# Performance work log

Measured on AMD Instinct MI355X. Metric: run time of the kernel, lower is better.

## Reference

```python
import jax, jax.numpy as jnp
import numpy as np

NUM_ENTS = 1000
NUM_RELS = 100
HIDDEN = 200
N_QUERY = 50000
N_HIST = 1000000
ALPHA = 0.5


def setup_inputs() -> dict:
    key = jax.random.key(0)
    ks = jax.random.split(key, 12)
    s = 0.05  # small init for numerical stability (xavier-like scale)
    return {
        "ent_emb": jax.random.normal(ks[0], (NUM_ENTS, HIDDEN), jnp.float32) * s,
        "rel_emb": jax.random.normal(ks[1], (NUM_RELS, HIDDEN), jnp.float32) * s,
        "tim_emb": jax.random.normal(ks[2], (1, HIDDEN), jnp.float32) * s,
        "g_w": jax.random.normal(ks[3], (3 * HIDDEN, HIDDEN), jnp.float32) * s,
        "g_b": jnp.zeros((HIDDEN,), jnp.float32),
        "c_w": jax.random.normal(ks[4], (3 * HIDDEN, HIDDEN), jnp.float32) * s,
        "c_b": jnp.zeros((HIDDEN,), jnp.float32),
        "hist_sub": jax.random.randint(ks[5], (N_HIST,), 0, NUM_ENTS, jnp.int32),
        "hist_rel": jax.random.randint(ks[6], (N_HIST,), 0, NUM_RELS, jnp.int32),
        "hist_obj": jax.random.randint(ks[7], (N_HIST,), 0, NUM_ENTS, jnp.int32),
        "sub": jax.random.randint(ks[8], (N_QUERY,), 0, NUM_ENTS, jnp.int32),
        "rel": jax.random.randint(ks[9], (N_QUERY,), 0, NUM_RELS, jnp.int32),
    }


def reference(ent_emb, rel_emb, tim_emb, g_w, g_b, c_w, c_b,
              hist_sub, hist_rel, hist_obj, sub, rel):
    E = ent_emb.shape[0]
    R = rel_emb.shape[0]
    N = sub.shape[0]
    # Triple-count histogram over all history graphs (fused scatter-add;
    # equivalent to the per-graph python loop vocab[s,r,o] += 1).
    vocab = jnp.zeros((E, R, E), jnp.float32).at[hist_sub, hist_rel, hist_obj].add(1.0)
    # Query features: [N, 3H]
    x = jnp.concatenate(
        [ent_emb[sub], rel_emb[rel], jnp.broadcast_to(tim_emb, (N, tim_emb.shape[1]))],
        axis=1)
    # Generate-mode score distribution
    gscore = jax.nn.softmax(x @ g_w + g_b, axis=1)  # [N, H]
    # Copy-mode mask: 1 where the (sub, rel) pair occurred in history
    mask = (vocab[sub, rel].sum(axis=1, keepdims=True) != 0).astype(x.dtype)  # [N, 1]
    cscore = jax.nn.softmax(jnp.tanh(x @ c_w + c_b) + mask, axis=1)  # [N, H]
    fscore = gscore + ALPHA * (cscore - gscore)
    return jnp.log(fscore)
```

## Files before the change

kernel.cpp:

```cpp
#include <hip/hip_runtime.h>
#include <math.h>

#define HIDDEN 200
#define LOG2E 1.4426950408889634f
#define LN2   0.6931471805599453f

typedef float f32x4 __attribute__((ext_vector_type(4)));

__global__ __launch_bounds__(256) void precompute_kernel(
    const float* __restrict__ ent, const float* __restrict__ rel,
    const float* __restrict__ tim,
    const float* __restrict__ g_w, const float* __restrict__ g_b,
    const float* __restrict__ c_w, const float* __restrict__ c_b,
    float* __restrict__ EA, float* __restrict__ EB) {
  const int mode = blockIdx.y;
  const float* w = mode ? c_w : g_w;
  const float* bias = mode ? c_b : g_b;
  const bool is_ent = blockIdx.x < 500;
  const int row0 = is_ent ? blockIdx.x * 2 : (blockIdx.x - 500) * 2;
  const float* in = is_ent ? ent : rel;
  const int k0 = is_ent ? 0 : 200;
  float* obase = is_ent ? (EA + row0 * 400 + mode * 200)
                        : (EB + row0 * 400 + mode * 200);

  __shared__ float a0[HIDDEN], a1[HIDDEN], tl[HIDDEN];
  const int c = threadIdx.x;
  if (c < HIDDEN) {
    a0[c] = in[row0 * HIDDEN + c];
    a1[c] = in[(row0 + 1) * HIDDEN + c];
    if (!is_ent) tl[c] = tim[c];
  }
  __syncthreads();
  if (c >= HIDDEN) return;

  const float* wp = w + k0 * HIDDEN + c;
  float acc0a = 0.f, acc0b = 0.f, acc1a = 0.f, acc1b = 0.f;
  #pragma unroll 4
  for (int k = 0; k < 100; ++k) {
    float w0 = wp[k * HIDDEN];
    float w1 = wp[(k + 100) * HIDDEN];
    acc0a += a0[k] * w0;
    acc0b += a0[k + 100] * w1;
    acc1a += a1[k] * w0;
    acc1b += a1[k + 100] * w1;
  }
  float r0 = acc0a + acc0b;
  float r1 = acc1a + acc1b;
  if (!is_ent) {
    const float* wt = w + 400 * HIDDEN + c;
    float ta = 0.f, tb = 0.f;
    #pragma unroll 4
    for (int k = 0; k < 100; ++k) {
      ta += tl[k] * wt[k * HIDDEN];
      tb += tl[k + 100] * wt[(k + 100) * HIDDEN];
    }
    float extra = ta + tb + bias[c];
    r0 += extra;
    r1 += extra;
  }
  if (mode == 0) {
    r0 = __builtin_amdgcn_exp2f(r0 * LOG2E);
    r1 = __builtin_amdgcn_exp2f(r1 * LOG2E);
  }
  obase[c] = r0;
  obase[400 + c] = r1;
}

__global__ __launch_bounds__(128) void pair_kernel(
    const float* __restrict__ EA, const float* __restrict__ EB,
    float* __restrict__ SG, float* __restrict__ SC) {
  const int s = blockIdx.x;
  __shared__ float row[400];
  for (int i = threadIdx.x; i < 400; i += 128) row[i] = EA[s * 400 + i];
  __syncthreads();
  const int r = threadIdx.x;
  if (r >= 100) return;

  const float* ebg = EB + r * 400;
  const float* ebc = ebg + 200;
  float sg = 0.f, sc = 0.f;
  #pragma unroll 4
  for (int k = 0; k < 200; ++k) {
    sg = fmaf(row[k], ebg[k], sg);
    float x = row[200 + k] + ebc[k];
    float e2 = __builtin_amdgcn_exp2f(x * (2.f * LOG2E));
    float th = (e2 - 1.f) * __builtin_amdgcn_rcpf(e2 + 1.f);
    sc += __builtin_amdgcn_exp2f(th * LOG2E);
  }
  SG[s * 100 + r] = sg;
  SC[s * 100 + r] = sc;
}

__global__ __launch_bounds__(256) void query_kernel(
    const float* __restrict__ EA, const float* __restrict__ EB,
    const float* __restrict__ SG, const float* __restrict__ SC,
    const int* __restrict__ sub, const int* __restrict__ rel,
    float* __restrict__ out, int total) {
  int t = blockIdx.x * blockDim.x + threadIdx.x;
  if (t >= total) return;
  unsigned q = (unsigned)t / 50u;
  unsigned j = (unsigned)t - q * 50u;

  int s = sub[q];
  int r = rel[q];
  float isg = 0.5f * __builtin_amdgcn_rcpf(SG[s * 100 + r]);
  float isc = 0.5f * __builtin_amdgcn_rcpf(SC[s * 100 + r]);

  const f32x4* ea = (const f32x4*)(EA + s * 400);
  const f32x4* eb = (const f32x4*)(EB + r * 400);
  f32x4 eg = ea[j] * eb[j];
  f32x4 xc = ea[j + 50] + eb[j + 50];

  f32x4 o;
  #pragma unroll
  for (int i = 0; i < 4; ++i) {
    float e2 = __builtin_amdgcn_exp2f(xc[i] * (2.f * LOG2E));
    float th = (e2 - 1.f) * __builtin_amdgcn_rcpf(e2 + 1.f);
    float ec = __builtin_amdgcn_exp2f(th * LOG2E);
    float v = fmaf(eg[i], isg, ec * isc);
    o[i] = __builtin_amdgcn_logf(v) * LN2;
  }
  __builtin_nontemporal_store(o, (f32x4*)out + t);
}

extern "C" void kernel_launch(void* const* d_in, const int* in_sizes, int n_in,
                              void* d_out, int out_size, void* d_ws, size_t ws_size,
                              hipStream_t stream) {
  const float* ent  = (const float*)d_in[0];
  const float* relE = (const float*)d_in[1];
  const float* tim  = (const float*)d_in[2];
  const float* g_w  = (const float*)d_in[3];
  const float* g_b  = (const float*)d_in[4];
  const float* c_w  = (const float*)d_in[5];
  const float* c_b  = (const float*)d_in[6];
  const int* sub = (const int*)d_in[10];
  const int* rel = (const int*)d_in[11];
  float* out = (float*)d_out;
  int N = in_sizes[10];

  float* ws = (float*)d_ws;
  float* EA = ws;
  float* EB = ws + 400000;
  float* SG = ws + 440000;
  float* SC = ws + 540000;

  dim3 grid1(550, 2);
  precompute_kernel<<<grid1, 256, 0, stream>>>(ent, relE, tim, g_w, g_b, c_w,
                                               c_b, EA, EB);
  pair_kernel<<<1000, 128, 0, stream>>>(EA, EB, SG, SC);

  int total = N * 50;
  int blocks = (total + 255) / 256;
  query_kernel<<<blocks, 256, 0, stream>>>(EA, EB, SG, SC, sub, rel, out,
                                           total);
}
```

Before: 141.8 us.

## Transpose relation table for coalesced pair kernel loads and split K across halves

```diff
diff --git a/kernel.cpp b/kernel.cpp
--- a/kernel.cpp
+++ b/kernel.cpp
@@ -12,7 +12,8 @@
     const float* __restrict__ tim,
     const float* __restrict__ g_w, const float* __restrict__ g_b,
     const float* __restrict__ c_w, const float* __restrict__ c_b,
-    float* __restrict__ EA, float* __restrict__ EB) {
+    float* __restrict__ EA, float* __restrict__ EB,
+    float* __restrict__ EBt) {
   const int mode = blockIdx.y;
   const float* w = mode ? c_w : g_w;
   const float* bias = mode ? c_b : g_b;
@@ -20,8 +21,6 @@
   const int row0 = is_ent ? blockIdx.x * 2 : (blockIdx.x - 500) * 2;
   const float* in = is_ent ? ent : rel;
   const int k0 = is_ent ? 0 : 200;
-  float* obase = is_ent ? (EA + row0 * 400 + mode * 200)
-                        : (EB + row0 * 400 + mode * 200);
 
   __shared__ float a0[HIDDEN], a1[HIDDEN], tl[HIDDEN];
   const int c = threadIdx.x;
@@ -62,33 +61,51 @@
     r0 = __builtin_amdgcn_exp2f(r0 * LOG2E);
     r1 = __builtin_amdgcn_exp2f(r1 * LOG2E);
   }
-  obase[c] = r0;
-  obase[400 + c] = r1;
+  const int col = mode * 200 + c;
+  if (is_ent) {
+    EA[row0 * 400 + col] = r0;
+    EA[(row0 + 1) * 400 + col] = r1;
+  } else {
+    EB[row0 * 400 + col] = r0;
+    EB[(row0 + 1) * 400 + col] = r1;
+    EBt[col * 100 + row0] = r0;
+    EBt[col * 100 + row0 + 1] = r1;
+  }
 }
 
-__global__ __launch_bounds__(128) void pair_kernel(
-    const float* __restrict__ EA, const float* __restrict__ EB,
+__global__ __launch_bounds__(256) void pair_kernel(
+    const float* __restrict__ EA, const float* __restrict__ EBt,
     float* __restrict__ SG, float* __restrict__ SC) {
   const int s = blockIdx.x;
   __shared__ float row[400];
-  for (int i = threadIdx.x; i < 400; i += 128) row[i] = EA[s * 400 + i];
+  __shared__ float psg[256], psc[256];
+  const int tid = threadIdx.x;
+  for (int i = tid; i < 400; i += 256) row[i] = EA[s * 400 + i];
   __syncthreads();
-  const int r = threadIdx.x;
-  if (r >= 100) return;
 
-  const float* ebg = EB + r * 400;
-  const float* ebc = ebg + 200;
+  const int half = tid >> 7;
+  const int r = tid & 127;
   float sg = 0.f, sc = 0.f;
-  #pragma unroll 4
-  for (int k = 0; k < 200; ++k) {
-    sg = fmaf(row[k], ebg[k], sg);
-    float x = row[200 + k] + ebc[k];
-    float e2 = __builtin_amdgcn_exp2f(x * (2.f * LOG2E));
-    float th = (e2 - 1.f) * __builtin_amdgcn_rcpf(e2 + 1.f);
-    sc += __builtin_amdgcn_exp2f(th * LOG2E);
+  if (r < 100) {
+    const int kbase = half * 100;
+    const float* tg = EBt + kbase * 100 + r;
+    const float* tc = EBt + (200 + kbase) * 100 + r;
+    #pragma unroll 4
+    for (int k = 0; k < 100; ++k) {
+      sg = fmaf(row[kbase + k], tg[k * 100], sg);
+      float x = row[200 + kbase + k] + tc[k * 100];
+      float e2 = __builtin_amdgcn_exp2f(x * (2.f * LOG2E));
+      float th = (e2 - 1.f) * __builtin_amdgcn_rcpf(e2 + 1.f);
+      sc += __builtin_amdgcn_exp2f(th * LOG2E);
+    }
   }
-  SG[s * 100 + r] = sg;
-  SC[s * 100 + r] = sc;
+  psg[tid] = sg;
+  psc[tid] = sc;
+  __syncthreads();
+  if (half == 0 && r < 100) {
+    SG[s * 100 + r] = psg[r] + psg[r + 128];
+    SC[s * 100 + r] = psc[r] + psc[r + 128];
+  }
 }
 
 __global__ __launch_bounds__(256) void query_kernel(
@@ -139,15 +156,16 @@
   int N = in_sizes[10];
 
   float* ws = (float*)d_ws;
-  float* EA = ws;
-  float* EB = ws + 400000;
-  float* SG = ws + 440000;
-  float* SC = ws + 540000;
+  float* EA  = ws;
+  float* EB  = ws + 400000;
+  float* EBt = ws + 440000;
+  float* SG  = ws + 480000;
+  float* SC  = ws + 580000;
 
   dim3 grid1(550, 2);
   precompute_kernel<<<grid1, 256, 0, stream>>>(ent, relE, tim, g_w, g_b, c_w,
-                                               c_b, EA, EB);
-  pair_kernel<<<1000, 128, 0, stream>>>(EA, EB, SG, SC);
+                                               c_b, EA, EB, EBt);
+  pair_kernel<<<1000, 256, 0, stream>>>(EA, EBt, SG, SC);
 
   int total = N * 50;
   int blocks = (total + 255) / 256;
```

After: 138.4 us. -2.4%, faster.
